# Kernel tuning notes

Measured on AMD Instinct MI355X. Metric: run time of the kernel, lower is better.

Reference implementation:

```python
import jax, jax.numpy as jnp
import numpy as np

B = 2
S0, S1, S2 = 1024, 256, 64
S = S0 + S1 + S2
H, KV, D = 16, 8, 128
H_VLM, H_EXP = 2048, 1024
F_VLM, F_EXP = 8192, 4096
EPS = 1e-6
ROPE_BASE = 1000000.0


def setup_inputs() -> dict:
    key = jax.random.key(0)
    ks = iter(jax.random.split(key, 64))

    def n(shape, scale=0.02):
        return jax.random.normal(next(ks), shape, jnp.float32) * scale

    inp = {}
    inp["x0"] = jax.random.normal(next(ks), (B, S0, H_VLM), jnp.float32)
    inp["x1"] = jax.random.normal(next(ks), (B, S1, H_EXP), jnp.float32)
    inp["x2"] = jax.random.normal(next(ks), (B, S2, H_EXP), jnp.float32)
    inp["attention_mask"] = jnp.zeros((B, 1, S, S), jnp.float32)
    inp["position_ids"] = jnp.broadcast_to(jnp.arange(S, dtype=jnp.int32), (B, S))
    for i, (hid, ffn) in enumerate([(H_VLM, F_VLM), (H_EXP, F_EXP), (H_EXP, F_EXP)]):
        p = f"e{i}_"
        inp[p + "ln1"] = jnp.ones((hid,), jnp.float32)
        inp[p + "ln2"] = jnp.ones((hid,), jnp.float32)
        inp[p + "wq"] = n((H * D, hid))
        inp[p + "wk"] = n((KV * D, hid))
        inp[p + "wv"] = n((KV * D, hid))
        inp[p + "wo"] = n((hid, H * D))
        inp[p + "qn"] = jnp.ones((D,), jnp.float32)
        inp[p + "kn"] = jnp.ones((D,), jnp.float32)
        inp[p + "wg"] = n((ffn, hid))
        inp[p + "wu"] = n((ffn, hid))
        inp[p + "wd"] = n((hid, ffn))
    return inp


def _rms(x, w):
    # Qwen3 RMSNorm (eps 1e-6), applied over the last dim
    return x * jax.lax.rsqrt(jnp.mean(x * x, axis=-1, keepdims=True) + EPS) * w


def _rope_cos_sin(pos):
    inv = 1.0 / (ROPE_BASE ** (jnp.arange(0, D, 2, dtype=jnp.float32) / D))
    freqs = pos.astype(jnp.float32)[..., None] * inv  # [B,S,D/2]
    emb = jnp.concatenate([freqs, freqs], axis=-1)  # [B,S,D]
    return jnp.cos(emb), jnp.sin(emb)


def _rot_half(x):
    x1, x2 = jnp.split(x, 2, axis=-1)
    return jnp.concatenate([-x2, x1], axis=-1)


def _forward(xs, params, attention_mask, position_ids):
    # Per-expert QKV projections with per-head q/k RMSNorm
    qs, ks, vs = [], [], []
    for x, p in zip(xs, params):
        ln1, ln2, wq, wk, wv, wo, qn, kn, wg, wu, wd = p
        h = _rms(x, ln1)
        b, s, _ = x.shape
        q = _rms(jnp.einsum('bsd,od->bso', h, wq).reshape(b, s, H, D), qn)
        k = _rms(jnp.einsum('bsd,od->bso', h, wk).reshape(b, s, KV, D), kn)
        v = jnp.einsum('bsd,od->bso', h, wv).reshape(b, s, KV, D)
        qs.append(q.transpose(0, 2, 1, 3))  # [B,H,s,D]
        ks.append(k.transpose(0, 2, 1, 3))
        vs.append(v.transpose(0, 2, 1, 3))
    # Joint cross-expert attention over concatenated sequence
    q = jnp.concatenate(qs, axis=2)  # [B,H,S,D]
    k = jnp.concatenate(ks, axis=2)  # [B,KV,S,D]
    v = jnp.concatenate(vs, axis=2)
    cos, sin = _rope_cos_sin(position_ids)
    cos, sin = cos[:, None], sin[:, None]  # unsqueeze head dim
    q = q * cos + _rot_half(q) * sin
    k = k * cos + _rot_half(k) * sin
    k = jnp.repeat(k, H // KV, axis=1)  # GQA repeat_kv
    v = jnp.repeat(v, H // KV, axis=1)
    scores = jnp.einsum('bhqd,bhkd->bhqk', q, k) * (D ** -0.5) + attention_mask
    probs = jax.nn.softmax(scores, axis=-1)
    att = jnp.einsum('bhqk,bhkd->bhqd', probs, v)
    att = att.transpose(0, 2, 1, 3).reshape(q.shape[0], -1, H * D)  # [B,S,H*D]
    # Split back per expert: o_proj + residual + post-LN + SwiGLU MLP + residual
    outs, start = [], 0
    for x, p in zip(xs, params):
        ln1, ln2, wq, wk, wv, wo, qn, kn, wg, wu, wd = p
        s = x.shape[1]
        o = jnp.einsum('bsi,oi->bso', att[:, start:start + s], wo) + x
        h = _rms(o, ln2)
        m = jax.nn.silu(jnp.einsum('bsd,fd->bsf', h, wg)) * jnp.einsum('bsd,fd->bsf', h, wu)
        outs.append(jnp.einsum('bsf,df->bsd', m, wd) + o)
        start += s
    return tuple(outs)


def reference(x0, x1, x2, attention_mask, position_ids,
              e0_ln1, e0_ln2, e0_wq, e0_wk, e0_wv, e0_wo, e0_qn, e0_kn, e0_wg, e0_wu, e0_wd,
              e1_ln1, e1_ln2, e1_wq, e1_wk, e1_wv, e1_wo, e1_qn, e1_kn, e1_wg, e1_wu, e1_wd,
              e2_ln1, e2_ln2, e2_wq, e2_wk, e2_wv, e2_wo, e2_qn, e2_kn, e2_wg, e2_wu, e2_wd):
    params = [
        (e0_ln1, e0_ln2, e0_wq, e0_wk, e0_wv, e0_wo, e0_qn, e0_kn, e0_wg, e0_wu, e0_wd),
        (e1_ln1, e1_ln2, e1_wq, e1_wk, e1_wv, e1_wo, e1_qn, e1_kn, e1_wg, e1_wu, e1_wd),
        (e2_ln1, e2_ln2, e2_wq, e2_wk, e2_wv, e2_wo, e2_qn, e2_kn, e2_wg, e2_wu, e2_wd),
    ]
    return _forward([x0, x1, x2], params, attention_mask, position_ids)
```

## Files before the change

### kernel.cpp

```cpp
#include <hip/hip_runtime.h>
#include <cstdint>
#include <cstddef>


using u16 = unsigned short;
typedef __attribute__((ext_vector_type(4))) float  f32x4;
typedef __attribute__((ext_vector_type(4))) u16    u16x4;
typedef __attribute__((ext_vector_type(8))) u16    u16x8;
typedef __attribute__((ext_vector_type(8))) short  s16x8;

__device__ __forceinline__ u16 f2bf(float f) {
  unsigned u = __builtin_bit_cast(unsigned, f);
  u = (u + 0x7FFF + ((u >> 16) & 1)) >> 16;
  return (u16)u;
}
__device__ __forceinline__ float bf2f(u16 h) {
  unsigned u = ((unsigned)h) << 16;
  return __builtin_bit_cast(float, u);
}
__device__ __forceinline__ f32x4 mfma16(s16x8 a, s16x8 b, f32x4 c) {
  return __builtin_amdgcn_mfma_f32_16x16x32_bf16(a, b, c, 0, 0, 0);
}
__device__ __forceinline__ void gl_lds16(const u16* g, u16* l) {
  __builtin_amdgcn_global_load_lds(
      (const __attribute__((address_space(1))) unsigned int*)g,
      (__attribute__((address_space(3))) unsigned int*)l, 16, 0, 0);
}

static constexpr size_t WB_OFF   = 0;
static constexpr size_t H1_OFF   = WB_OFF   + 201326592;
static constexpr size_t H2_OFF   = H1_OFF   + 9699328;
static constexpr size_t QKV_OFF  = H2_OFF   + 9699328;
static constexpr size_t QB_OFF   = QKV_OFF  + 22020096;
static constexpr size_t KB_OFF   = QB_OFF   + 11010048;
static constexpr size_t VT_OFF   = KB_OFF   + 5505024;
static constexpr size_t ATTO_OFF = VT_OFF   + 5505024;
static constexpr size_t GU_OFF   = ATTO_OFF + 11010048;
static constexpr size_t WS_NEED  = GU_OFF   + 77594624;

struct CastTab { const float* src[15]; int pre[16]; };
struct DstoArg { size_t v[15]; };

__global__ __launch_bounds__(256) void cast_weights2(CastTab tab, DstoArg dsto,
                                                     u16* __restrict__ dst) {
  int c = blockIdx.x;
  int a = 0;
  while (c >= tab.pre[a + 1]) a++;
  const f32x4* s = (const f32x4*)(tab.src[a] + ((size_t)(c - tab.pre[a]) << 15));
  u16x4* d = (u16x4*)(dst + dsto.v[a] + (((size_t)(c - tab.pre[a])) << 15));
  int t = threadIdx.x;
  for (int i = t; i < 8192; i += 256) {
    f32x4 v = s[i];
    u16x4 o; o[0] = f2bf(v[0]); o[1] = f2bf(v[1]); o[2] = f2bf(v[2]); o[3] = f2bf(v[3]);
    d[i] = o;
  }
}

__global__ __launch_bounds__(256) void cast_gu_all(
    const float* __restrict__ g0, const float* __restrict__ u0,
    const float* __restrict__ g1, const float* __restrict__ u1,
    const float* __restrict__ g2, const float* __restrict__ u2,
    u16* __restrict__ dst, size_t o0, size_t o1, size_t o2) {
  const long N0 = 8388608, N1 = 10485760, N2 = 12582912;
  long i = (long)blockIdx.x * 256 + threadIdx.x;
  long stride = (long)gridDim.x * 256;
  for (; i < N2; i += stride) {
    const float* g; const float* u; u16* d; int logh; long li;
    if (i < N0)      { g = g0; u = u0; d = dst + o0; logh = 11; li = i; }
    else if (i < N1) { g = g1; u = u1; d = dst + o1; logh = 10; li = i - N0; }
    else             { g = g2; u = u2; d = dst + o2; logh = 10; li = i - N1; }
    int hid = 1 << logh;
    long e4 = li << 2;
    long r = e4 >> logh;
    int  k = (int)(e4 & (hid - 1));
    long super = r >> 6; int sub = (int)(r & 63);
    const float* src = (sub < 32 ? g + ((super << 5) + sub) * (long)hid
                                 : u + ((super << 5) + (sub - 32)) * (long)hid) + k;
    f32x4 v = *(const f32x4*)src;
    u16x4 o; o[0] = f2bf(v[0]); o[1] = f2bf(v[1]); o[2] = f2bf(v[2]); o[3] = f2bf(v[3]);
    ((u16x4*)d)[li] = o;
  }
}

__global__ __launch_bounds__(256) void rms_all(
    const float* __restrict__ i0, const float* __restrict__ i1, const float* __restrict__ i2,
    const float* __restrict__ w0, const float* __restrict__ w1, const float* __restrict__ w2,
    u16* __restrict__ out) {
  int row = blockIdx.x;
  const float* xr; const float* wr; size_t oo; int hid;
  if (row < 2048)      { xr = i0 + (size_t)row * 2048; wr = w0; oo = (size_t)row * 2048; hid = 2048; }
  else if (row < 2560) { int r = row - 2048; xr = i1 + (size_t)r * 1024; wr = w1;
                         oo = 4194304 + (size_t)r * 1024; hid = 1024; }
  else                 { int r = row - 2560; xr = i2 + (size_t)r * 1024; wr = w2;
                         oo = 4718592 + (size_t)r * 1024; hid = 1024; }
  const f32x4* x4 = (const f32x4*)xr;
  const f32x4* w4 = (const f32x4*)wr;
  int n4 = hid >> 2;
  int t = threadIdx.x;
  float ss = 0.f;
  for (int i = t; i < n4; i += 256) {
    f32x4 v = x4[i];
    ss += v[0] * v[0] + v[1] * v[1] + v[2] * v[2] + v[3] * v[3];
  }
#pragma unroll
  for (int m = 1; m < 64; m <<= 1) ss += __shfl_xor(ss, m);
  __shared__ float part[4];
  if ((t & 63) == 0) part[t >> 6] = ss;
  __syncthreads();
  float tot = part[0] + part[1] + part[2] + part[3];
  float rs = rsqrtf(tot / (float)hid + 1e-6f);
  u16x4* orow = (u16x4*)(out + oo);
  for (int i = t; i < n4; i += 256) {
    f32x4 v = x4[i];
    f32x4 g = w4[i];
    u16x4 o;
    o[0] = f2bf(v[0] * rs * g[0]); o[1] = f2bf(v[1] * rs * g[1]);
    o[2] = f2bf(v[2] * rs * g[2]); o[3] = f2bf(v[3] * rs * g[3]);
    orow[i] = o;
  }
}

template <int MB, int N0>
__device__ __forceinline__ void mmblk(f32x4 (&acc)[8][4], const s16x8 (&afr)[2][4],
                                      const s16x8 (&bfr)[2][4]) {
#pragma unroll
  for (int ks = 0; ks < 2; ks++)
#pragma unroll
    for (int j = 0; j < 4; j++)
#pragma unroll
      for (int ni = 0; ni < 2; ni++)
        acc[MB + j][N0 + ni] =
            mfma16(afr[ks][j], bfr[ks][N0 + ni], acc[MB + j][N0 + ni]);
}

#define GB256_BAR() do { __builtin_amdgcn_sched_barrier(0); \
                         __builtin_amdgcn_s_barrier(); } while (0)
#define GB256_LGKM0() do { asm volatile("s_waitcnt lgkmcnt(0)" ::: "memory"); \
                           __builtin_amdgcn_sched_barrier(0); } while (0)

template <int RESID, int OUTBF, bool SPLIT, bool SILU>
__global__ __launch_bounds__(512, 2) void gemm256(
    const u16* __restrict__ A, int Astride, int logSe, int bstride, int rowoff,
    const u16* __restrict__ Bw, int K, int kLen, int N,
    void* __restrict__ C, const float* __restrict__ R, size_t mn) {
  __shared__ u16 As[2][256 * 64];
  __shared__ u16 Bs[2][256 * 64];
  const int t = threadIdx.x;

  int gx = gridDim.x, nwg = gx * gridDim.y;
  int flat = blockIdx.y * gx + blockIdx.x;
  int q = nwg >> 3, r8 = nwg & 7;
  int xcd = flat & 7, idx = flat >> 3;
  int nf = (xcd < r8 ? xcd * (q + 1) : r8 * (q + 1) + (xcd - r8) * q) + idx;
  const int nt = (nf % gx) * 256, mt = (nf / gx) * 256;

  const int w = t >> 6, l = t & 63;
  const int wm = (w >> 2) * 128, wn = (w & 3) * 64;
  const int l15 = l & 15, lg = l >> 4;
  const int sr8 = t >> 3, u8 = t & 7;
  const int mask_se = (1 << logSe) - 1;
  const int k0 = SPLIT ? (int)blockIdx.z * kLen : 0;
  const int kLast = k0 + kLen - 64;

  f32x4 acc[8][4];
#pragma unroll
  for (int i = 0; i < 8; i++)
#pragma unroll
    for (int j = 0; j < 4; j++) acc[i][j] = (f32x4){0.f, 0.f, 0.f, 0.f};

  auto stA = [&](int c, int qb, int ktv) {
    int row = qb + sr8;
    int gr = mt + row;
    int grow = ((gr >> logSe) * bstride) + (gr & mask_se) + rowoff;
    int su = u8 ^ (row & 7);
    gl_lds16(A + (size_t)grow * Astride + ktv + su * 8, &As[c][row * 64 + u8 * 8]);
  };
  auto stB = [&](int c, int half, int pair, int ktv) {
    int row = (pair * 2 + (t >> 8)) * 64 + half * 32 + ((t & 255) >> 3);
    int su = u8 ^ (row & 7);
    gl_lds16(Bw + (size_t)(nt + row) * K + ktv + su * 8, &Bs[c][row * 64 + u8 * 8]);
  };
  auto rdA = [&](int c, int mi, int ks) -> s16x8 {
    int row = wm + mi * 16 + l15;
    int u = ks * 4 + lg;
    return *(const s16x8*)&As[c][row * 64 + (u ^ (row & 7)) * 8];
  };
  auto rdB = [&](int c, int ni, int ks) -> s16x8 {
    int row = wn + ni * 16 + l15;
    int u = ks * 4 + lg;
    return *(const s16x8*)&Bs[c][row * 64 + (u ^ (row & 7)) * 8];
  };

  {
    int kt1 = k0 + 64;
    stA(0, 0, k0); stA(0, 128, k0);
    stB(0, 0, 0, k0); stB(0, 0, 1, k0);
    stB(0, 1, 0, k0); stB(0, 1, 1, k0);
    stA(0, 64, k0); stA(0, 192, k0);
    stA(1, 0, kt1); stA(1, 128, kt1);
    stB(1, 0, 0, kt1); stB(1, 0, 1, kt1);
    stB(1, 1, 0, kt1); stB(1, 1, 1, kt1);
    stA(1, 64, kt1); stA(1, 192, kt1);
  }
  asm volatile("s_waitcnt vmcnt(12)" ::: "memory");
  GB256_BAR();

  s16x8 afr[2][4], bfr[2][4];
  int c = 0;
  for (int kt0 = k0; kt0 < k0 + kLen; kt0 += 64) {
    int ktp = kt0 + 128 <= kLast ? kt0 + 128 : kLast;
#pragma unroll
    for (int ks = 0; ks < 2; ks++) {
#pragma unroll
      for (int j = 0; j < 4; j++) afr[ks][j] = rdA(c, j, ks);
#pragma unroll
      for (int j = 0; j < 2; j++) bfr[ks][j] = rdB(c, j, ks);
    }
    GB256_BAR();
    GB256_LGKM0();
    __builtin_amdgcn_s_setprio(1);
    mmblk<0, 0>(acc, afr, bfr);
    __builtin_amdgcn_s_setprio(0);
    asm volatile("s_waitcnt vmcnt(10)" ::: "memory");
    GB256_BAR();
#pragma unroll
    for (int ks = 0; ks < 2; ks++)
#pragma unroll
      for (int j = 2; j < 4; j++) bfr[ks][j] = rdB(c, j, ks);
    stA(c, 0, ktp); stA(c, 128, ktp);
    stB(c, 0, 0, ktp); stB(c, 0, 1, ktp);
    GB256_BAR();
    GB256_LGKM0();
    __builtin_amdgcn_s_setprio(1);
    mmblk<0, 2>(acc, afr, bfr);
    __builtin_amdgcn_s_setprio(0);
    asm volatile("s_waitcnt vmcnt(12)" ::: "memory");
    GB256_BAR();
#pragma unroll
    for (int ks = 0; ks < 2; ks++)
#pragma unroll
      for (int j = 0; j < 4; j++) afr[ks][j] = rdA(c, 4 + j, ks);
    stB(c, 1, 0, ktp); stB(c, 1, 1, ktp);
    GB256_BAR();
    GB256_LGKM0();
    __builtin_amdgcn_s_setprio(1);
    mmblk<4, 0>(acc, afr, bfr);
    __builtin_amdgcn_s_setprio(0);
    GB256_BAR();
    stA(c, 64, ktp); stA(c, 192, ktp);
    __builtin_amdgcn_s_setprio(1);
    mmblk<4, 2>(acc, afr, bfr);
    __builtin_amdgcn_s_setprio(0);
    asm volatile("s_waitcnt vmcnt(12)" ::: "memory");
    GB256_BAR();
    c ^= 1;
  }
  asm volatile("s_waitcnt vmcnt(0)" ::: "memory");

  float* Pz = SPLIT ? ((float*)C + (size_t)blockIdx.z * mn) : nullptr;
#pragma unroll
  for (int mi = 0; mi < 8; mi++) {
#pragma unroll
    for (int r = 0; r < 4; r++) {
      int crow = mt + wm + mi * 16 + lg * 4 + r;
      if (SILU) {
        size_t rb = (size_t)crow * (N >> 1);
        int super = (nt + wn) >> 6;
#pragma unroll
        for (int ni = 0; ni < 2; ni++) {
          int col = super * 32 + ni * 16 + l15;
          float g = acc[mi][ni][r], u = acc[mi][ni + 2][r];
          float s = g / (1.f + __expf(-g));
          ((u16*)C)[rb + col] = f2bf(s * u);
        }
      } else {
        size_t rb = (size_t)crow * N;
#pragma unroll
        for (int ni = 0; ni < 4; ni++) {
          int col = nt + wn + ni * 16 + l15;
          float v = acc[mi][ni][r];
          if (SPLIT) {
            Pz[rb + col] = v;
          } else {
            if (RESID == 1) v += R[rb + col];
            if (RESID == 2) v += ((const float*)C)[rb + col];
            if (OUTBF) ((u16*)C)[rb + col] = f2bf(v);
            else       ((float*)C)[rb + col] = v;
          }
        }
      }
    }
  }
}

struct GSeg {
  const u16* A; const u16* Bw; float* C;
  int Astride, logSe, bstride, rowoff;
  int K, kLen, N, nx, ntiles;
  size_t mn;
};
struct GJobs { GSeg s[2]; int cum[3]; };

__global__ __launch_bounds__(256) void gemm_jobs(GJobs J) {
  const int t = threadIdx.x;
  int flat = blockIdx.x;
  int si = (flat >= J.cum[1]) ? 1 : 0;
  const GSeg g = J.s[si];
  int local = flat - J.cum[si];
  int z = local / g.ntiles;
  int tl = local - z * g.ntiles;
  int count = g.ntiles;
  int q = count >> 3, r8 = count & 7;
  int xcd = tl & 7, idx = tl >> 3;
  int nf = (xcd < r8 ? xcd * (q + 1) : r8 * (q + 1) + (xcd - r8) * q) + idx;
  const int nt = nf % g.nx, mt = nf / g.nx;
  const int k0 = z * g.kLen;

  __shared__ u16 As[128 * 64];
  __shared__ u16 Bs[128 * 64];
  const int w = t >> 6, l = t & 63;
  const int wr = (w >> 1) * 64, wc = (w & 1) * 64;
  const int l15 = l & 15, lg = l >> 4;
  f32x4 acc[4][4];
#pragma unroll
  for (int i = 0; i < 4; i++)
#pragma unroll
    for (int j = 0; j < 4; j++) acc[i][j] = (f32x4){0.f, 0.f, 0.f, 0.f};

  const int sr = t >> 3, su0 = t & 7;
  const int mask_se = (1 << g.logSe) - 1;
  const int k1 = k0 + g.kLen;

  for (int kt = k0; kt < k1; kt += 64) {
    __syncthreads();
#pragma unroll
    for (int i = 0; i < 4; i++) {
      int row = i * 32 + sr;
      int gr = mt * 128 + row;
      int grow = ((gr >> g.logSe) * g.bstride) + (gr & mask_se) + g.rowoff;
      int su = su0 ^ (row & 7);
      gl_lds16(g.A + (size_t)grow * g.Astride + kt + su * 8, &As[row * 64 + su0 * 8]);
    }
#pragma unroll
    for (int i = 0; i < 4; i++) {
      int row = i * 32 + sr;
      int gc = nt * 128 + row;
      int su = su0 ^ (row & 7);
      gl_lds16(g.Bw + (size_t)gc * g.K + kt + su * 8, &Bs[row * 64 + su0 * 8]);
    }
    __syncthreads();

    s16x8 af[2][4], bfr[2][4];
#pragma unroll
    for (int mi = 0; mi < 4; mi++) {
      int row = wr + mi * 16 + l15;
#pragma unroll
      for (int ks = 0; ks < 2; ks++) {
        int u = ks * 4 + lg;
        af[ks][mi] = *(const s16x8*)&As[row * 64 + (u ^ (row & 7)) * 8];
      }
    }
#pragma unroll
    for (int ni = 0; ni < 4; ni++) {
      int row = wc + ni * 16 + l15;
#pragma unroll
      for (int ks = 0; ks < 2; ks++) {
        int u = ks * 4 + lg;
        bfr[ks][ni] = *(const s16x8*)&Bs[row * 64 + (u ^ (row & 7)) * 8];
      }
    }
#pragma unroll
    for (int ks = 0; ks < 2; ks++)
#pragma unroll
      for (int mi = 0; mi < 4; mi++)
#pragma unroll
        for (int ni = 0; ni < 4; ni++)
          acc[mi][ni] = mfma16(af[ks][mi], bfr[ks][ni], acc[mi][ni]);
  }

  float* Pz = g.C + (size_t)z * g.mn;
#pragma unroll
  for (int mi = 0; mi < 4; mi++) {
#pragma unroll
    for (int r = 0; r < 4; r++) {
      int crow = mt * 128 + wr + mi * 16 + lg * 4 + r;
      size_t rb = (size_t)crow * g.N;
#pragma unroll
      for (int ni = 0; ni < 4; ni++) {
        int col = nt * 128 + wc + ni * 16 + l15;
        Pz[rb + col] = acc[mi][ni][r];
      }
    }
  }
}

struct RSeg3 { const float* part; float* C; const float* R; int nz; size_t mn4; int nb; };
struct R3 { RSeg3 s[3]; };

template <int MODE>
__global__ __launch_bounds__(256) void reduce3(R3 J) {
  int b = blockIdx.x, si = 0, base = 0;
  while (si < 2 && b >= base + J.s[si].nb) { base += J.s[si].nb; si++; }
  RSeg3 g = J.s[si];
  const f32x4* p4 = (const f32x4*)g.part;
  for (size_t i = (size_t)(b - base) * 256 + threadIdx.x; i < g.mn4;
       i += (size_t)g.nb * 256) {
    f32x4 s = p4[i];
    for (int z = 1; z < g.nz; z++) s += p4[(size_t)z * g.mn4 + i];
    if (MODE == 1) s += ((const f32x4*)g.R)[i];
    else           s += ((const f32x4*)g.C)[i];
    ((f32x4*)g.C)[i] = s;
  }
}

struct RSegS { const float* part; u16* mout; int nz; size_t mnF4; int F4; size_t mnPart; int nb; };
struct RS2 { RSegS s[2]; };

__global__ __launch_bounds__(256) void reduce_silu2(RS2 J) {
  int b = blockIdx.x, si = 0, base = 0;
  if (b >= J.s[0].nb) { base = J.s[0].nb; si = 1; }
  RSegS g = J.s[si];
  for (size_t i = (size_t)(b - base) * 256 + threadIdx.x; i < g.mnF4;
       i += (size_t)g.nb * 256) {
    size_t row = i / g.F4;
    int cm4 = (int)(i - row * g.F4) * 4;
    int super = cm4 >> 5, j = cm4 & 31;
    size_t gb = row * (size_t)(g.F4 * 8) + (size_t)super * 64 + j;
    f32x4 gg = *(const f32x4*)(g.part + gb);
    f32x4 uu = *(const f32x4*)(g.part + gb + 32);
    for (int z = 1; z < g.nz; z++) {
      gg += *(const f32x4*)(g.part + (size_t)z * g.mnPart + gb);
      uu += *(const f32x4*)(g.part + (size_t)z * g.mnPart + gb + 32);
    }
    u16x4 o;
#pragma unroll
    for (int k = 0; k < 4; k++) {
      float s = gg[k] / (1.f + __expf(-gg[k]));
      o[k] = f2bf(s * uu[k]);
    }
    *(u16x4*)(g.mout + row * (size_t)(g.F4 * 4) + cm4) = o;
  }
}

__global__ __launch_bounds__(256) void qk_rope(
    const float* __restrict__ pe0, const float* __restrict__ pe1,
    const float* __restrict__ pe2,
    const float* __restrict__ qn0, const float* __restrict__ qn1, const float* __restrict__ qn2,
    const float* __restrict__ kn0, const float* __restrict__ kn1, const float* __restrict__ kn2,
    const int* __restrict__ pos, u16* __restrict__ Q, u16* __restrict__ K) {
  int tk = blockIdx.x;
  int b = tk / 1344, sg = tk % 1344;
  int w = threadIdx.x >> 6, l = threadIdx.x & 63;
  int hr = blockIdx.y * 4 + w;
  int e, off, Se;
  if (sg < 1024)      { e = 0; off = 0;    Se = 1024; }
  else if (sg < 1280) { e = 1; off = 1024; Se = 256;  }
  else                { e = 2; off = 1280; Se = 64;   }
  int r = b * Se + (sg - off);
  const float* P; size_t mn; int nz;
  if (e == 0)      { P = pe0; mn = 8388608; nz = 2; }
  else if (e == 1) { P = pe1; mn = 2097152; nz = 2; }
  else             { P = pe2; mn = 524288;  nz = 4; }
  size_t base = (size_t)r * 4096;
  int c0; const float* nw; u16* dst;
  if (hr < 16) {
    c0 = hr * 128 + l;
    nw = (e == 0) ? qn0 : (e == 1) ? qn1 : qn2;
    dst = Q + ((size_t)(b * 16 + hr) * 1344 + sg) * 128;
  } else {
    int kh = hr - 16;
    c0 = 2048 + kh * 128 + l;
    nw = (e == 0) ? kn0 : (e == 1) ? kn1 : kn2;
    dst = K + ((size_t)(b * 8 + kh) * 1344 + sg) * 128;
  }
  float x0v = 0.f, x1v = 0.f;
  for (int z = 0; z < nz; z++) {
    const float* pz = P + (size_t)z * mn + base;
    x0v += pz[c0];
    x1v += pz[c0 + 64];
  }
  float ss = x0v * x0v + x1v * x1v;
#pragma unroll
  for (int m = 1; m < 64; m <<= 1) ss += __shfl_xor(ss, m);
  float rs = rsqrtf(ss * (1.f / 128.f) + 1e-6f);
  float y0 = x0v * rs * nw[l], y1 = x1v * rs * nw[l + 64];
  float p = (float)pos[b * 1344 + sg];
  float inv = exp2f(-(float)l * 0.3114307588956902f);
  float th = p * inv;
  float cz = __cosf(th), sz = __sinf(th);
  dst[l]      = f2bf(y0 * cz - y1 * sz);
  dst[l + 64] = f2bf(y1 * cz + y0 * sz);
}

__global__ __launch_bounds__(256) void v_trans(
    const float* __restrict__ pe0, const float* __restrict__ pe1,
    const float* __restrict__ pe2, u16* __restrict__ Vt) {
  __shared__ u16 tile[64][72];
  int st = blockIdx.x;
  int b = st / 21, s0 = (st % 21) * 64;
  int kvh = blockIdx.y >> 1, dh = (blockIdx.y & 1) * 64;
  int t = threadIdx.x;
  int sl = t >> 2, d0 = (t & 3) * 16;
  int sg = s0 + sl;
  int e, off, Se;
  if (sg < 1024)      { e = 0; off = 0;    Se = 1024; }
  else if (sg < 1280) { e = 1; off = 1024; Se = 256;  }
  else                { e = 2; off = 1280; Se = 64;   }
  int r = b * Se + (sg - off);
  const float* P; size_t mn; int nz;
  if (e == 0)      { P = pe0; mn = 8388608; nz = 2; }
  else if (e == 1) { P = pe1; mn = 2097152; nz = 2; }
  else             { P = pe2; mn = 524288;  nz = 4; }
  size_t base = (size_t)r * 4096 + 3072 + kvh * 128 + dh + d0;
  float a16[16];
#pragma unroll
  for (int j = 0; j < 16; j++) a16[j] = 0.f;
  for (int z = 0; z < nz; z++) {
    const f32x4* p4 = (const f32x4*)(P + (size_t)z * mn + base);
#pragma unroll
    for (int q4 = 0; q4 < 4; q4++) {
      f32x4 v = p4[q4];
      a16[q4 * 4 + 0] += v[0]; a16[q4 * 4 + 1] += v[1];
      a16[q4 * 4 + 2] += v[2]; a16[q4 * 4 + 3] += v[3];
    }
  }
#pragma unroll
  for (int j = 0; j < 16; j++) tile[sl][d0 + j] = f2bf(a16[j]);
  __syncthreads();
  int dl = t >> 2, sb = (t & 3) * 16;
  u16* dst = Vt + ((size_t)(b * 8 + kvh) * 128 + dh + dl) * 1344 + s0 + sb;
  u16x8 o0, o1;
#pragma unroll
  for (int j = 0; j < 8; j++) { o0[j] = tile[sb + j][dl]; o1[j] = tile[sb + 8 + j][dl]; }
  *(u16x8*)dst = o0;
  *(u16x8*)(dst + 8) = o1;
}

__global__ __launch_bounds__(256, 3) void attn(
    const u16* __restrict__ Q, const u16* __restrict__ K, const u16* __restrict__ Vt,
    u16* __restrict__ attO) {
  constexpr int S = 1344;
  __shared__ u16 Qs[64 * 128];
  __shared__ u16 Ks[64 * 128];
  __shared__ u16 Vts[128 * 64];
  u16 (*Ps)[16 * 64] = (u16 (*)[16 * 64])Qs;
  int bh = blockIdx.y;
  int b = bh >> 4, h = bh & 15, kvh = h >> 1;
  int q0 = blockIdx.x * 64;
  int t = threadIdx.x, w = t >> 6, l = t & 63;
  const int l15 = l & 15, lg = l >> 4;
  const u16* Qg = Q + ((size_t)(b * 16 + h) * S + q0) * 128;
  const u16* Kg = K + ((size_t)(b * 8 + kvh) * S) * 128;
  const u16* Vg = Vt + ((size_t)(b * 8 + kvh) * 128) * S;

  {
    int unit = t & 15, r16 = t >> 4;
#pragma unroll
    for (int i = 0; i < 4; i++) {
      int row = i * 16 + r16;
      int su = (unit & 8) | ((unit & 7) ^ (row & 7));
      gl_lds16(Qg + (size_t)row * 128 + su * 8, &Qs[row * 128 + unit * 8]);
    }
  }
  __syncthreads();
  s16x8 qf[4];
  {
    int qrow = w * 16 + l15;
#pragma unroll
    for (int ks = 0; ks < 4; ks++) {
      int u = ks * 4 + lg;
      int su = (u & 8) | ((u & 7) ^ (qrow & 7));
      qf[ks] = *(const s16x8*)&Qs[qrow * 128 + su * 8];
    }
  }

  float mrow[4] = {-3e38f, -3e38f, -3e38f, -3e38f};
  float lrow[4] = {0.f, 0.f, 0.f, 0.f};
  f32x4 of[8];
#pragma unroll
  for (int d = 0; d < 8; d++) of[d] = (f32x4){0.f, 0.f, 0.f, 0.f};
  const float scale = 0.08838834764831845f;

  for (int kt = 0; kt < 21; ++kt) {
    int k0 = kt * 64;
    __syncthreads();
    {
      int unit = t & 15, r16 = t >> 4;
#pragma unroll
      for (int i = 0; i < 4; i++) {
        int row = i * 16 + r16;
        int su = (unit & 8) | ((unit & 7) ^ (row & 7));
        gl_lds16(Kg + (size_t)(k0 + row) * 128 + su * 8, &Ks[row * 128 + unit * 8]);
      }
      int u8 = t & 7, r32 = t >> 3;
#pragma unroll
      for (int i = 0; i < 4; i++) {
        int row = i * 32 + r32;
        int su = u8 ^ (row & 7);
        gl_lds16(Vg + (size_t)row * S + k0 + su * 8, &Vts[row * 64 + u8 * 8]);
      }
    }
    __syncthreads();

    f32x4 sf[4];
    __builtin_amdgcn_s_setprio(1);
#pragma unroll
    for (int cb = 0; cb < 4; cb++) {
      f32x4 a = (f32x4){0.f, 0.f, 0.f, 0.f};
      int krow = cb * 16 + l15;
#pragma unroll
      for (int ks = 0; ks < 4; ks++) {
        int u = ks * 4 + lg;
        int su = (u & 8) | ((u & 7) ^ (krow & 7));
        s16x8 kf = *(const s16x8*)&Ks[krow * 128 + su * 8];
        a = mfma16(qf[ks], kf, a);
      }
      sf[cb] = a;
    }
    __builtin_amdgcn_s_setprio(0);

    float pv[4][4], tmax[4];
#pragma unroll
    for (int r = 0; r < 4; r++) {
      float v0 = sf[0][r] * scale;
      float v1 = sf[1][r] * scale;
      float v2 = sf[2][r] * scale;
      float v3 = sf[3][r] * scale;
      pv[0][r] = v0; pv[1][r] = v1; pv[2][r] = v2; pv[3][r] = v3;
      tmax[r] = fmaxf(fmaxf(v0, v1), fmaxf(v2, v3));
    }
#pragma unroll
    for (int m = 1; m < 16; m <<= 1)
#pragma unroll
      for (int r = 0; r < 4; r++) tmax[r] = fmaxf(tmax[r], __shfl_xor(tmax[r], m));

    int need = 0;
#pragma unroll
    for (int r = 0; r < 4; r++) need |= (tmax[r] > mrow[r] + 8.f) ? 1 : 0;
    if (__any(need)) {
      float fr[4];
#pragma unroll
      for (int r = 0; r < 4; r++) {
        float mnew = fmaxf(mrow[r], tmax[r]);
        fr[r] = __expf(mrow[r] - mnew);
        mrow[r] = mnew;
        lrow[r] *= fr[r];
      }
#pragma unroll
      for (int d = 0; d < 8; d++)
#pragma unroll
        for (int r = 0; r < 4; r++) of[d][r] *= fr[r];
    }
#pragma unroll
    for (int r = 0; r < 4; r++) {
      float rs = 0.f;
#pragma unroll
      for (int cb = 0; cb < 4; cb++) { pv[cb][r] = __expf(pv[cb][r] - mrow[r]); rs += pv[cb][r]; }
#pragma unroll
      for (int m = 1; m < 16; m <<= 1) rs += __shfl_xor(rs, m);
      lrow[r] += rs;
    }

#pragma unroll
    for (int cb = 0; cb < 4; cb++)
#pragma unroll
      for (int r = 0; r < 4; r++) {
        int prow = lg * 4 + r;
        int col = cb * 16 + l15;
        int su = (col >> 3) ^ (prow & 7);
        Ps[w][prow * 64 + su * 8 + (col & 7)] = f2bf(pv[cb][r]);
      }
    __syncthreads();

    s16x8 pa[2];
#pragma unroll
    for (int ks = 0; ks < 2; ks++) {
      int prow = l15;
      int u = ks * 4 + lg;
      pa[ks] = *(const s16x8*)&Ps[w][prow * 64 + (u ^ (prow & 7)) * 8];
    }
    __builtin_amdgcn_s_setprio(1);
#pragma unroll
    for (int d = 0; d < 8; d++) {
      int vrow = d * 16 + l15;
#pragma unroll
      for (int ks = 0; ks < 2; ks++) {
        int u = ks * 4 + lg;
        s16x8 vf = *(const s16x8*)&Vts[vrow * 64 + (u ^ (vrow & 7)) * 8];
        of[d] = mfma16(pa[ks], vf, of[d]);
      }
    }
    __builtin_amdgcn_s_setprio(0);
  }

#pragma unroll
  for (int r = 0; r < 4; r++) {
    float il = 1.f / lrow[r];
    int sg = q0 + w * 16 + lg * 4 + r;
    u16* orow = attO + ((size_t)(b * S + sg)) * 2048 + h * 128;
#pragma unroll
    for (int d = 0; d < 8; d++) orow[d * 16 + l15] = f2bf(of[d][r] * il);
  }
}

extern "C" void kernel_launch(void* const* d_in, const int* in_sizes, int n_in,
                              void* d_out, int out_size, void* d_ws, size_t ws_size,
                              hipStream_t stream) {
  if (ws_size < WS_NEED) return;

  const float* x[3] = {(const float*)d_in[0], (const float*)d_in[1], (const float*)d_in[2]};
  const int* pos = (const int*)d_in[4];
  auto W = [&](int e, int k) -> const float* { return (const float*)d_in[5 + e * 11 + k]; };

  char* ws = (char*)d_ws;
  u16* wbf  = (u16*)(ws + WB_OFF);
  u16* h1   = (u16*)(ws + H1_OFF);
  u16* h2   = (u16*)(ws + H2_OFF);
  u16* Qb   = (u16*)(ws + QB_OFF);
  u16* Kb   = (u16*)(ws + KB_OFF);
  u16* Vtb  = (u16*)(ws + VT_OFF);
  u16* attO = (u16*)(ws + ATTO_OFF);
  u16* m    = (u16*)(ws + GU_OFF);
  float* scrA = (float*)(ws + GU_OFF);
  float* scrC = (float*)(ws + H1_OFF);
  float* dout = (float*)d_out;

  const int hid[3] = {2048, 1024, 1024}, ffn[3] = {8192, 4096, 4096};
  const size_t douto[3] = {0, 4194304, 4718592};
  const size_t mo[3]    = {0, 16777216, 18874368};

  size_t woff[3][7];
  CastTab tab;
  DstoArg dsarg;
  {
    size_t cum = 0; int cc = 0, ci = 0;
    for (int e = 0; e < 3; e++) {
      const size_t sz[7] = {(size_t)2048 * hid[e], (size_t)1024 * hid[e], (size_t)1024 * hid[e],
                            (size_t)2048 * hid[e], (size_t)ffn[e] * hid[e],
                            (size_t)ffn[e] * hid[e], (size_t)ffn[e] * hid[e]};
      const int kidx[7] = {2, 3, 4, 5, 8, 9, 10};
      for (int j = 0; j < 7; j++) {
        woff[e][j] = cum;
        if (j != 4 && j != 5) {
          tab.src[ci] = W(e, kidx[j]);
          tab.pre[ci] = cc;
          dsarg.v[ci] = cum;
          cc += (int)(sz[j] >> 15);
          ci++;
        }
        cum += sz[j];
      }
    }
    tab.pre[15] = cc;
  }

  cast_weights2<<<dim3(1536), dim3(256), 0, stream>>>(tab, dsarg, wbf);
  cast_gu_all<<<dim3(2048), dim3(256), 0, stream>>>(
      W(0, 8), W(0, 9), W(1, 8), W(1, 9), W(2, 8), W(2, 9),
      wbf, woff[0][4], woff[1][4], woff[2][4]);

  rms_all<<<dim3(2688), dim3(256), 0, stream>>>(
      x[0], x[1], x[2], W(0, 0), W(1, 0), W(2, 0), h1);

  float* qp1 = (float*)(ws + QKV_OFF);
  float* qp2 = (float*)(ws + H2_OFF);
  gemm256<0, 0, true, false><<<dim3(16, 8, 2), dim3(512), 0, stream>>>(
      h1, 2048, 11, 0, 0, wbf + woff[0][0], 2048, 1024, 4096, scrA, nullptr,
      (size_t)8388608);
  {
    GJobs J = {};
    J.s[0] = {h1 + douto[1], wbf + woff[1][0], qp1, 1024, 9, 0, 0,
              1024, 512, 4096, 32, 128, (size_t)2097152};
    J.s[1] = {h1 + douto[2], wbf + woff[2][0], qp2, 1024, 7, 0, 0,
              1024, 256, 4096, 32, 32, (size_t)524288};
    J.cum[0] = 0; J.cum[1] = 256; J.cum[2] = 384;
    gemm_jobs<<<dim3(384), dim3(256), 0, stream>>>(J);
  }

  qk_rope<<<dim3(2688, 6), dim3(256), 0, stream>>>(
      scrA, qp1, qp2, W(0, 6), W(1, 6), W(2, 6), W(0, 7), W(1, 7), W(2, 7),
      pos, Qb, Kb);
  v_trans<<<dim3(42, 16), dim3(256), 0, stream>>>(scrA, qp1, qp2, Vtb);

  attn<<<dim3(21, 32), dim3(256), 0, stream>>>(Qb, Kb, Vtb, attO);

  gemm256<0, 0, true, false><<<dim3(8, 8, 4), dim3(512), 0, stream>>>(
      attO, 2048, 10, 1344, 0, wbf + woff[0][3], 2048, 512, 2048, scrA, nullptr,
      (size_t)4194304);
  {
    float* p1 = (float*)(ws + QKV_OFF);
    float* p2 = (float*)(ws + QKV_OFF + 16777216);
    GJobs J = {};
    J.s[0] = {attO, wbf + woff[1][3], p1, 2048, 8, 1344, 1024,
              2048, 256, 1024, 8, 32, (size_t)524288};
    J.s[1] = {attO, wbf + woff[2][3], p2, 2048, 6, 1344, 1280,
              2048, 128, 1024, 8, 8, (size_t)131072};
    J.cum[0] = 0; J.cum[1] = 256; J.cum[2] = 384;
    gemm_jobs<<<dim3(384), dim3(256), 0, stream>>>(J);
    R3 R = {};
    R.s[0] = {scrA, dout, x[0], 4, 1048576, 1536};
    R.s[1] = {p1, dout + douto[1], x[1], 8, 131072, 192};
    R.s[2] = {p2, dout + douto[2], x[2], 16, 32768, 48};
    reduce3<1><<<dim3(1776), dim3(256), 0, stream>>>(R);
  }

  rms_all<<<dim3(2688), dim3(256), 0, stream>>>(
      dout, dout + douto[1], dout + douto[2], W(0, 1), W(1, 1), W(2, 1), h2);

  gemm256<0, 0, false, true><<<dim3(64, 8), dim3(512), 0, stream>>>(
      h2, 2048, 11, 0, 0, wbf + woff[0][4], 2048, 2048, 16384, m, nullptr, 0);
  {
    float* p1 = (float*)(ws + QKV_OFF);
    float* p2 = (float*)(ws + QKV_OFF + 33554432);
    GJobs J = {};
    J.s[0] = {h2 + douto[1], wbf + woff[1][4], p1, 1024, 9, 0, 0,
              1024, 512, 8192, 64, 256, (size_t)4194304};
    J.s[1] = {h2 + douto[2], wbf + woff[2][4], p2, 1024, 7, 0, 0,
              1024, 256, 8192, 64, 64, (size_t)1048576};
    J.cum[0] = 0; J.cum[1] = 512; J.cum[2] = 768;
    gemm_jobs<<<dim3(768), dim3(256), 0, stream>>>(J);
    RS2 R = {};
    R.s[0] = {p1, m + mo[1], 2, 524288, 1024, 4194304, 2048};
    R.s[1] = {p2, m + mo[2], 4, 131072, 1024, 1048576, 512};
    reduce_silu2<<<dim3(2560), dim3(256), 0, stream>>>(R);
  }

  gemm256<0, 0, true, false><<<dim3(8, 8, 4), dim3(512), 0, stream>>>(
      m, 8192, 11, 0, 0, wbf + woff[0][6], 8192, 2048, 2048, scrC, nullptr,
      (size_t)4194304);
  {
    float* p1 = (float*)(ws + GU_OFF + 38797312);
    float* p2 = (float*)(ws + GU_OFF + 38797312 + 16777216);
    GJobs J = {};
    J.s[0] = {m + mo[1], wbf + woff[1][6], p1, 4096, 9, 0, 0,
              4096, 512, 1024, 8, 32, (size_t)524288};
    J.s[1] = {m + mo[2], wbf + woff[2][6], p2, 4096, 7, 0, 0,
              4096, 256, 1024, 8, 8, (size_t)131072};
    J.cum[0] = 0; J.cum[1] = 256; J.cum[2] = 384;
    gemm_jobs<<<dim3(384), dim3(256), 0, stream>>>(J);
    R3 R = {};
    R.s[0] = {scrC, dout, nullptr, 4, 1048576, 1536};
    R.s[1] = {p1, dout + douto[1], nullptr, 8, 131072, 192};
    R.s[2] = {p2, dout + douto[2], nullptr, 16, 32768, 48};
    reduce3<2><<<dim3(1776), dim3(256), 0, stream>>>(R);
  }
}
```

Measured before the change: 689.9 us.

## Single-buffer LDS tiles in 256x256 GEMM to raise occupancy

Replaces double-buffered A/B shared-memory tiles with a single buffer that is refilled in place, region by region, as each region is consumed. This halves LDS usage so two workgroups can fit per CU. The cost is a shorter prefetch distance of one tile and tighter vmcnt waits, so global load latency may be less hidden and ordering hazards are more likely.

```diff
diff --git a/kernel.cpp b/kernel.cpp
--- a/kernel.cpp
+++ b/kernel.cpp
@@ -143,8 +143,8 @@
     const u16* __restrict__ A, int Astride, int logSe, int bstride, int rowoff,
     const u16* __restrict__ Bw, int K, int kLen, int N,
     void* __restrict__ C, const float* __restrict__ R, size_t mn) {
-  __shared__ u16 As[2][256 * 64];
-  __shared__ u16 Bs[2][256 * 64];
+  __shared__ u16 As[256 * 64];
+  __shared__ u16 Bs[256 * 64];
   const int t = threadIdx.x;
 
   int gx = gridDim.x, nwg = gx * gridDim.y;
@@ -168,92 +168,83 @@
 #pragma unroll
     for (int j = 0; j < 4; j++) acc[i][j] = (f32x4){0.f, 0.f, 0.f, 0.f};
 
-  auto stA = [&](int c, int qb, int ktv) {
+  auto stA = [&](int qb, int ktv) {
     int row = qb + sr8;
     int gr = mt + row;
     int grow = ((gr >> logSe) * bstride) + (gr & mask_se) + rowoff;
     int su = u8 ^ (row & 7);
-    gl_lds16(A + (size_t)grow * Astride + ktv + su * 8, &As[c][row * 64 + u8 * 8]);
+    gl_lds16(A + (size_t)grow * Astride + ktv + su * 8, &As[row * 64 + u8 * 8]);
   };
-  auto stB = [&](int c, int half, int pair, int ktv) {
+  auto stB = [&](int half, int pair, int ktv) {
     int row = (pair * 2 + (t >> 8)) * 64 + half * 32 + ((t & 255) >> 3);
     int su = u8 ^ (row & 7);
-    gl_lds16(Bw + (size_t)(nt + row) * K + ktv + su * 8, &Bs[c][row * 64 + u8 * 8]);
+    gl_lds16(Bw + (size_t)(nt + row) * K + ktv + su * 8, &Bs[row * 64 + u8 * 8]);
   };
-  auto rdA = [&](int c, int mi, int ks) -> s16x8 {
+  auto rdA = [&](int mi, int ks) -> s16x8 {
     int row = wm + mi * 16 + l15;
     int u = ks * 4 + lg;
-    return *(const s16x8*)&As[c][row * 64 + (u ^ (row & 7)) * 8];
+    return *(const s16x8*)&As[row * 64 + (u ^ (row & 7)) * 8];
   };
-  auto rdB = [&](int c, int ni, int ks) -> s16x8 {
+  auto rdB = [&](int ni, int ks) -> s16x8 {
     int row = wn + ni * 16 + l15;
     int u = ks * 4 + lg;
-    return *(const s16x8*)&Bs[c][row * 64 + (u ^ (row & 7)) * 8];
+    return *(const s16x8*)&Bs[row * 64 + (u ^ (row & 7)) * 8];
   };
 
-  {
-    int kt1 = k0 + 64;
-    stA(0, 0, k0); stA(0, 128, k0);
-    stB(0, 0, 0, k0); stB(0, 0, 1, k0);
-    stB(0, 1, 0, k0); stB(0, 1, 1, k0);
-    stA(0, 64, k0); stA(0, 192, k0);
-    stA(1, 0, kt1); stA(1, 128, kt1);
-    stB(1, 0, 0, kt1); stB(1, 0, 1, kt1);
-    stB(1, 1, 0, kt1); stB(1, 1, 1, kt1);
-    stA(1, 64, kt1); stA(1, 192, kt1);
-  }
-  asm volatile("s_waitcnt vmcnt(12)" ::: "memory");
+  stA(0, k0); stA(128, k0);
+  stB(0, 0, k0); stB(0, 1, k0);
+  stB(1, 0, k0); stB(1, 1, k0);
+  stA(64, k0); stA(192, k0);
+  asm volatile("s_waitcnt vmcnt(4)" ::: "memory");
   GB256_BAR();
 
   s16x8 afr[2][4], bfr[2][4];
-  int c = 0;
   for (int kt0 = k0; kt0 < k0 + kLen; kt0 += 64) {
-    int ktp = kt0 + 128 <= kLast ? kt0 + 128 : kLast;
+    int ktp = (kt0 + 64 <= kLast) ? kt0 + 64 : kLast;
 #pragma unroll
     for (int ks = 0; ks < 2; ks++) {
 #pragma unroll
-      for (int j = 0; j < 4; j++) afr[ks][j] = rdA(c, j, ks);
-#pragma unroll
-      for (int j = 0; j < 2; j++) bfr[ks][j] = rdB(c, j, ks);
+      for (int j = 0; j < 4; j++) afr[ks][j] = rdA(j, ks);
+#pragma unroll
+      for (int j = 0; j < 2; j++) bfr[ks][j] = rdB(j, ks);
     }
     GB256_BAR();
     GB256_LGKM0();
     __builtin_amdgcn_s_setprio(1);
     mmblk<0, 0>(acc, afr, bfr);
     __builtin_amdgcn_s_setprio(0);
-    asm volatile("s_waitcnt vmcnt(10)" ::: "memory");
+    asm volatile("s_waitcnt vmcnt(2)" ::: "memory");
     GB256_BAR();
 #pragma unroll
     for (int ks = 0; ks < 2; ks++)
 #pragma unroll
-      for (int j = 2; j < 4; j++) bfr[ks][j] = rdB(c, j, ks);
-    stA(c, 0, ktp); stA(c, 128, ktp);
-    stB(c, 0, 0, ktp); stB(c, 0, 1, ktp);
+      for (int j = 2; j < 4; j++) bfr[ks][j] = rdB(j, ks);
+    stA(0, ktp); stA(128, ktp);
+    stB(0, 0, ktp); stB(0, 1, ktp);
     GB256_BAR();
     GB256_LGKM0();
     __builtin_amdgcn_s_setprio(1);
     mmblk<0, 2>(acc, afr, bfr);
     __builtin_amdgcn_s_setprio(0);
-    asm volatile("s_waitcnt vmcnt(12)" ::: "memory");
+    asm volatile("s_waitcnt vmcnt(4)" ::: "memory");
     GB256_BAR();
 #pragma unroll
     for (int ks = 0; ks < 2; ks++)
 #pragma unroll
-      for (int j = 0; j < 4; j++) afr[ks][j] = rdA(c, 4 + j, ks);
-    stB(c, 1, 0, ktp); stB(c, 1, 1, ktp);
+      for (int j = 0; j < 4; j++) afr[ks][j] = rdA(4 + j, ks);
+    stB(1, 0, ktp); stB(1, 1, ktp);
     GB256_BAR();
     GB256_LGKM0();
     __builtin_amdgcn_s_setprio(1);
     mmblk<4, 0>(acc, afr, bfr);
     __builtin_amdgcn_s_setprio(0);
     GB256_BAR();
-    stA(c, 64, ktp); stA(c, 192, ktp);
+    stA(64, ktp); stA(192, ktp);
     __builtin_amdgcn_s_setprio(1);
     mmblk<4, 2>(acc, afr, bfr);
     __builtin_amdgcn_s_setprio(0);
-    asm volatile("s_waitcnt vmcnt(12)" ::: "memory");
+    asm volatile("s_waitcnt vmcnt(4)" ::: "memory");
     GB256_BAR();
-    c ^= 1;
   }
   asm volatile("s_waitcnt vmcnt(0)" ::: "memory");
 
```

New measurement: 690.1 us. No clear change (+0.0%).
